# Performance work log

Measured on AMD Instinct MI355X. Metric: run time of the kernel, lower is better.

Reference implementation:

```python
import jax, jax.numpy as jnp
from jax import lax
import numpy as np

B, T, H, C = 64, 512, 1024, 21


def setup_inputs() -> dict:
    key = jax.random.key(0)
    k1, k2, k3, k4 = jax.random.split(key, 4)
    return {
        "sequence_output": jax.random.normal(k1, (B, T, H), dtype=jnp.float32),
        "input_mask": jax.random.randint(k2, (B, T), 0, 2, dtype=jnp.int32),
        "W": jax.random.normal(k3, (H, C), dtype=jnp.float32) * 0.02,
        "b": jnp.zeros((C,), dtype=jnp.float32),
        "transitions": jax.random.normal(k4, (C, C), dtype=jnp.float32) * 0.1,
    }


def crf_decode(logits, transitions, seq_len):
    """Viterbi decode matching tfa.text.crf_decode semantics (length-masked)."""
    Bb, Tt, Cc = logits.shape
    ident = jnp.arange(Cc, dtype=jnp.int32)[None, :]  # identity backpointers

    def fwd_step(state, inp):
        logit_t, t = inp  # [B,C], scalar step index
        scores = state[:, :, None] + transitions[None, :, :]  # [B, C_prev, C_cur]
        bp = jnp.argmax(scores, axis=1).astype(jnp.int32)      # [B, C]
        new_state = jnp.max(scores, axis=1) + logit_t          # [B, C]
        valid = (t < seq_len)[:, None]                          # [B, 1]
        state = jnp.where(valid, new_state, state)
        bp = jnp.where(valid, bp, ident)
        return state, bp

    ts = jnp.arange(1, Tt)
    xs = (jnp.transpose(logits[:, 1:], (1, 0, 2)), ts)
    final_state, bps = lax.scan(fwd_step, logits[:, 0], xs)  # bps: [T-1, B, C]
    last_tag = jnp.argmax(final_state, axis=-1).astype(jnp.int32)  # [B]

    def back_step(tag, bp_t):
        tag = jnp.take_along_axis(bp_t, tag[:, None], axis=1)[:, 0]
        return tag, tag

    _, tags_rev = lax.scan(back_step, last_tag, bps, reverse=True)  # [T-1, B]
    tags = jnp.concatenate([tags_rev, last_tag[None, :]], axis=0)   # [T, B]
    return jnp.transpose(tags, (1, 0))  # [B, T]


def reference(sequence_output, input_mask, W, b, transitions):
    # classifier logits
    logits = jnp.einsum("bth,hc->btc", sequence_output, W) + b  # [B,T,C]
    mask = (input_mask == 1).astype(jnp.int32)
    seq_len = jnp.sum(mask, axis=-1)  # [B]
    decode_tags = crf_decode(logits, transitions, seq_len)
    return jax.nn.one_hot(decode_tags, logits.shape[-1], dtype=jnp.float32), logits
```

## Files before the change

kernel.cpp:

```cpp
#include <hip/hip_runtime.h>
#include <stdint.h>

#define BB 64
#define TT 512
#define HH 1024
#define CC 21

#define GAS __attribute__((address_space(1)))
#define LAS __attribute__((address_space(3)))
__device__ __forceinline__ void gll16(const void* g, void* l) {
    __builtin_amdgcn_global_load_lds((const GAS uint32_t*)g, (LAS uint32_t*)l, 16, 0, 0);
}

#define RL(x, lane) __uint_as_float(__builtin_amdgcn_readlane(__float_as_uint(x), (lane)))

__global__ __launch_bounds__(512) void logits_kernel(
    const float* __restrict__ seq,
    const float* __restrict__ W,
    const float* __restrict__ bias,
    float* __restrict__ logits)
{
    __shared__ float comb[7][128][22];

    const int t = threadIdx.x;
    const int w = t >> 6;
    const int l = t & 63;
    const int row0 = blockIdx.x * 128;
    const int h0 = w * 128;

    const float* x0 = seq + (size_t)(row0 + l) * HH + h0;
    const float* x1 = seq + (size_t)(row0 + l + 64) * HH + h0;
    const float* wb = W + (size_t)h0 * CC;

    float acc0[CC], acc1[CC];
#pragma unroll
    for (int c = 0; c < CC; ++c) { acc0[c] = 0.f; acc1[c] = 0.f; }

    float4 xa[4], xbv[4], xan[4], xbn[4];
    float wr[6], wrn[6];

#pragma unroll
    for (int k = 0; k < 4; ++k) {
        xa[k]  = *(const float4*)(x0 + k * 4);
        xbv[k] = *(const float4*)(x1 + k * 4);
    }
#pragma unroll
    for (int i = 0; i < 6; ++i) {
        int j = i * 64 + l;
        wr[i] = (j < 16 * CC) ? wb[j] : 0.f;
    }

#pragma unroll 2
    for (int ch = 0; ch < 8; ++ch) {
        if (ch < 7) {
            const float* px0 = x0 + (ch + 1) * 16;
            const float* px1 = x1 + (ch + 1) * 16;
#pragma unroll
            for (int k = 0; k < 4; ++k) {
                xan[k] = *(const float4*)(px0 + k * 4);
                xbn[k] = *(const float4*)(px1 + k * 4);
            }
            const float* pw = wb + (ch + 1) * 16 * CC;
#pragma unroll
            for (int i = 0; i < 6; ++i) {
                int j = i * 64 + l;
                wrn[i] = (j < 16 * CC) ? pw[j] : 0.f;
            }
        }

#pragma unroll
        for (int g = 0; g < 4; ++g) {
#pragma unroll
            for (int j = 0; j < 4; ++j) {
                float xv0 = (&xa[g].x)[j];
                float xv1 = (&xbv[g].x)[j];
#pragma unroll
                for (int c = 0; c < CC; ++c) {
                    const int idx = (g * 4 + j) * CC + c;
                    float s = RL(wr[idx >> 6], idx & 63);
                    acc0[c] = fmaf(s, xv0, acc0[c]);
                    acc1[c] = fmaf(s, xv1, acc1[c]);
                }
            }
        }

        if (ch < 7) {
#pragma unroll
            for (int k = 0; k < 4; ++k) { xa[k] = xan[k]; xbv[k] = xbn[k]; }
#pragma unroll
            for (int i = 0; i < 6; ++i) wr[i] = wrn[i];
        }
    }

    if (w > 0) {
#pragma unroll
        for (int c = 0; c < CC; ++c) {
            comb[w - 1][l][c]      = acc0[c];
            comb[w - 1][l + 64][c] = acc1[c];
        }
    }
    __syncthreads();
    if (w == 0) {
        float* o0 = logits + (size_t)(row0 + l) * CC;
        float* o1 = logits + (size_t)(row0 + l + 64) * CC;
#pragma unroll
        for (int c = 0; c < CC; ++c) {
            float s0 = acc0[c] + bias[c];
            float s1 = acc1[c] + bias[c];
#pragma unroll
            for (int i = 0; i < 7; ++i) {
                s0 += comb[i][l][c];
                s1 += comb[i][l + 64][c];
            }
            o0[c] = s0;
            o1[c] = s1;
        }
    }
}

__global__ __launch_bounds__(256) void viterbi_kernel(
    const float* __restrict__ logits,
    const int* __restrict__ mask,
    const float* __restrict__ trans,
    float* __restrict__ onehot)
{
    __shared__ __align__(16) float lg[(TT + 1) * CC];
    __shared__ float stS[TT * CC];
    __shared__ float trL[CC * CC];
    __shared__ unsigned char bp[TT * CC];
    __shared__ unsigned char tagl[TT];
    __shared__ unsigned char mapl[12 * CC];
    __shared__ unsigned char bnd[13];

    const int tid = threadIdx.x;
    const int w = tid >> 6;
    const int l = tid & 63;
    const int b = blockIdx.x;

    const float* lb = logits + (size_t)b * TT * CC;
    for (int i = w; i < 42; i += 4)
        gll16(lb + (size_t)(i * 64 + l) * 4, &lg[i * 256]);

    for (int j = tid; j < CC * CC; j += 256) trL[j] = trans[j];

    int sl = 0;
#pragma unroll
    for (int k = 0; k < 8; ++k) sl += mask[b * TT + k * 64 + l];
#pragma unroll
    for (int o = 32; o > 0; o >>= 1) sl += __shfl_xor(sl, o);
    const int idstart = (sl >= 1) ? (sl - 1) : 0;

    asm volatile("s_waitcnt vmcnt(0)" ::: "memory");
    __syncthreads();

    if (w == 0) {
        const bool act = (l < CC);
        const int cc = act ? l : 0;
        float tcol[CC];
#pragma unroll
        for (int cp = 0; cp < CC; ++cp) tcol[cp] = trL[cp * CC + cc];

        float st = lg[cc];
        if (act) stS[l] = st;
        float lgt_next = lg[CC + cc];

#pragma unroll 1
        for (int t = 1; t < sl; ++t) {
            float lgt = lgt_next;
            lgt_next = lg[(t + 1) * CC + cc];
            float sc[CC];
#pragma unroll
            for (int cp = 0; cp < CC; ++cp) sc[cp] = RL(st, cp) + tcol[cp];
            float m0 = fmaxf(fmaxf(sc[0], sc[1]), sc[2]);
            float m1 = fmaxf(fmaxf(sc[3], sc[4]), sc[5]);
            float m2 = fmaxf(fmaxf(sc[6], sc[7]), sc[8]);
            float m3 = fmaxf(fmaxf(sc[9], sc[10]), sc[11]);
            float m4 = fmaxf(fmaxf(sc[12], sc[13]), sc[14]);
            float m5 = fmaxf(fmaxf(sc[15], sc[16]), sc[17]);
            float m6 = fmaxf(fmaxf(sc[18], sc[19]), sc[20]);
            float n0 = fmaxf(fmaxf(m0, m1), m2);
            float n1 = fmaxf(fmaxf(m3, m4), m5);
            float best = fmaxf(fmaxf(n0, n1), m6);
            st = best + lgt;
            if (act) stS[t * CC + l] = st;
        }

        float fs[CC];
#pragma unroll
        for (int cp = 0; cp < CC; ++cp) fs[cp] = RL(st, cp);
        float q0 = fmaxf(fmaxf(fs[0], fs[1]), fs[2]);
        float q1 = fmaxf(fmaxf(fs[3], fs[4]), fs[5]);
        float q2 = fmaxf(fmaxf(fs[6], fs[7]), fs[8]);
        float q3 = fmaxf(fmaxf(fs[9], fs[10]), fs[11]);
        float q4 = fmaxf(fmaxf(fs[12], fs[13]), fs[14]);
        float q5 = fmaxf(fmaxf(fs[15], fs[16]), fs[17]);
        float q6 = fmaxf(fmaxf(fs[18], fs[19]), fs[20]);
        float fbest = fmaxf(fmaxf(fmaxf(q0, q1), fmaxf(q2, q3)),
                            fmaxf(fmaxf(q4, q5), q6));
        int e[CC];
#pragma unroll
        for (int cp = 0; cp < CC; ++cp) e[cp] = (fs[cp] == fbest) ? cp : 63;
        int i0 = min(min(e[0], e[1]), e[2]);
        int i1 = min(min(e[3], e[4]), e[5]);
        int i2 = min(min(e[6], e[7]), e[8]);
        int i3 = min(min(e[9], e[10]), e[11]);
        int i4 = min(min(e[12], e[13]), e[14]);
        int i5 = min(min(e[15], e[16]), e[17]);
        int i6 = min(min(e[18], e[19]), e[20]);
        int last = min(min(min(i0, i1), min(i2, i3)), min(min(i4, i5), i6));
        if (l == 0) tagl[TT - 1] = (unsigned char)last;
    } else {
        int s = (w - 1) * 64 + l;
        if (s < 189) {
            int c0 = s % CC, prow = s / CC;
#pragma unroll 1
            for (int p = idstart + prow; p < TT; p += 9)
                bp[p * CC + c0] = (unsigned char)c0;
        }
    }
    __syncthreads();

    if (tid < 252) {
        const int c0 = tid % CC, tg = tid / CC;
        float tc[CC];
#pragma unroll
        for (int cp = 0; cp < CC; ++cp) tc[cp] = trL[cp * CC + c0];
#pragma unroll 1
        for (int t = 1 + tg; t < sl; t += 12) {
            const float* sp = stS + (t - 1) * CC;
            float bv = sp[0] + tc[0];
            int bi = 0;
#pragma unroll
            for (int cp = 1; cp < CC; ++cp) {
                float v = sp[cp] + tc[cp];
                bool g = v > bv;
                bv = g ? v : bv;
                bi = g ? cp : bi;
            }
            bp[(t - 1) * CC + c0] = (unsigned char)bi;
        }
    }
    __syncthreads();

    if (tid < 252) {
        int g = tid / CC, cand = tid % CC;
        int endp = g * 43;
        int startp = min(g * 43 + 42, TT - 2);
        int m = cand;
#pragma unroll 1
        for (int i = 0; i < 43; ++i) {
            int p = startp - i;
            int pr = (p >= endp) ? p : endp;
            int m2 = bp[pr * CC + m];
            m = (p >= endp) ? m2 : m;
        }
        mapl[g * CC + cand] = (unsigned char)m;
    }
    __syncthreads();

    if (tid == 0) {
        int eb = tagl[TT - 1];
        bnd[12] = (unsigned char)eb;
        for (int g = 11; g >= 0; --g) {
            eb = mapl[g * CC + eb];
            bnd[g] = (unsigned char)eb;
        }
    }
    __syncthreads();

    if (tid < 12) {
        int g = tid;
        int endp = g * 43;
        int startp = min(g * 43 + 42, TT - 2);
        int eb = bnd[g + 1];
#pragma unroll 1
        for (int p = startp; p >= endp; --p) {
            eb = bp[p * CC + eb];
            tagl[p] = (unsigned char)eb;
        }
    }
    __syncthreads();

    if (tid < 252) {
        const int c0 = tid % CC, prow = tid / CC;
        float* ob = onehot + (size_t)b * TT * CC;
#pragma unroll 1
        for (int p = prow; p < TT; p += 12)
            ob[(size_t)p * CC + c0] = (c0 == (int)tagl[p]) ? 1.f : 0.f;
    }
}

extern "C" void kernel_launch(void* const* d_in, const int* in_sizes, int n_in,
                              void* d_out, int out_size, void* d_ws, size_t ws_size,
                              hipStream_t stream) {
    const float* seq   = (const float*)d_in[0];
    const int*   msk   = (const int*)d_in[1];
    const float* W     = (const float*)d_in[2];
    const float* bias  = (const float*)d_in[3];
    const float* trans = (const float*)d_in[4];

    float* onehot_out = (float*)d_out;
    float* logits_out = onehot_out + (size_t)BB * TT * CC;

    logits_kernel<<<256, 512, 0, stream>>>(seq, W, bias, logits_out);
    viterbi_kernel<<<BB, 256, 0, stream>>>(logits_out, msk, trans, onehot_out);
}
```

Measured before the change: 135.0 us.

## Split logits GEMV across hidden halves and sum partials in viterbi kernel

The logits kernel now launches twice as many blocks, each covering half of the hidden dimension, so the GPU gets 512 workgroups instead of 256. The second half's partial sums go to a workspace buffer. The viterbi kernel loads both partials, adds them in LDS and writes the final logits out. This aims to improve CU utilisation for the bandwidth-bound GEMV. In exchange it adds extra global traffic for the partial buffer and more load work in the serial viterbi kernel. A fallback path runs the original kernel when the workspace is too small.

```diff
diff --git a/kernel.cpp b/kernel.cpp
--- a/kernel.cpp
+++ b/kernel.cpp
@@ -14,19 +14,22 @@
 
 #define RL(x, lane) __uint_as_float(__builtin_amdgcn_readlane(__float_as_uint(x), (lane)))
 
-__global__ __launch_bounds__(512) void logits_kernel(
+__global__ __launch_bounds__(512) void logits_split_kernel(
     const float* __restrict__ seq,
     const float* __restrict__ W,
     const float* __restrict__ bias,
-    float* __restrict__ logits)
+    float* __restrict__ outA,
+    float* __restrict__ outB)
 {
     __shared__ float comb[7][128][22];
 
     const int t = threadIdx.x;
     const int w = t >> 6;
     const int l = t & 63;
-    const int row0 = blockIdx.x * 128;
-    const int h0 = w * 128;
+    const int r  = blockIdx.x >> 1;
+    const int hb = blockIdx.x & 1;
+    const int row0 = r * 128;
+    const int h0 = hb * 512 + w * 64;
 
     const float* x0 = seq + (size_t)(row0 + l) * HH + h0;
     const float* x1 = seq + (size_t)(row0 + l + 64) * HH + h0;
@@ -51,8 +54,8 @@
     }
 
 #pragma unroll 2
-    for (int ch = 0; ch < 8; ++ch) {
-        if (ch < 7) {
+    for (int ch = 0; ch < 4; ++ch) {
+        if (ch < 3) {
             const float* px0 = x0 + (ch + 1) * 16;
             const float* px1 = x1 + (ch + 1) * 16;
 #pragma unroll
@@ -84,7 +87,7 @@
             }
         }
 
-        if (ch < 7) {
+        if (ch < 3) {
 #pragma unroll
             for (int k = 0; k < 4; ++k) { xa[k] = xan[k]; xbv[k] = xbn[k]; }
 #pragma unroll
@@ -101,6 +104,103 @@
     }
     __syncthreads();
     if (w == 0) {
+        float* dst = hb ? outB : outA;
+        float* o0 = dst + (size_t)(row0 + l) * CC;
+        float* o1 = dst + (size_t)(row0 + l + 64) * CC;
+#pragma unroll
+        for (int c = 0; c < CC; ++c) {
+            float s0 = acc0[c] + (hb ? 0.f : bias[c]);
+            float s1 = acc1[c] + (hb ? 0.f : bias[c]);
+#pragma unroll
+            for (int i = 0; i < 7; ++i) {
+                s0 += comb[i][l][c];
+                s1 += comb[i][l + 64][c];
+            }
+            o0[c] = s0;
+            o1[c] = s1;
+        }
+    }
+}
+
+__global__ __launch_bounds__(512) void logits_full_kernel(
+    const float* __restrict__ seq, const float* __restrict__ W,
+    const float* __restrict__ bias, float* __restrict__ logits)
+{
+    __shared__ float comb[7][128][22];
+    const int t = threadIdx.x;
+    const int w = t >> 6;
+    const int l = t & 63;
+    const int row0 = blockIdx.x * 128;
+    const int h0 = w * 128;
+
+    const float* x0 = seq + (size_t)(row0 + l) * HH + h0;
+    const float* x1 = seq + (size_t)(row0 + l + 64) * HH + h0;
+    const float* wb = W + (size_t)h0 * CC;
+
+    float acc0[CC], acc1[CC];
+#pragma unroll
+    for (int c = 0; c < CC; ++c) { acc0[c] = 0.f; acc1[c] = 0.f; }
+
+    float4 xa[4], xbv[4], xan[4], xbn[4];
+    float wr[6], wrn[6];
+#pragma unroll
+    for (int k = 0; k < 4; ++k) {
+        xa[k]  = *(const float4*)(x0 + k * 4);
+        xbv[k] = *(const float4*)(x1 + k * 4);
+    }
+#pragma unroll
+    for (int i = 0; i < 6; ++i) {
+        int j = i * 64 + l;
+        wr[i] = (j < 16 * CC) ? wb[j] : 0.f;
+    }
+#pragma unroll 2
+    for (int ch = 0; ch < 8; ++ch) {
+        if (ch < 7) {
+            const float* px0 = x0 + (ch + 1) * 16;
+            const float* px1 = x1 + (ch + 1) * 16;
+#pragma unroll
+            for (int k = 0; k < 4; ++k) {
+                xan[k] = *(const float4*)(px0 + k * 4);
+                xbn[k] = *(const float4*)(px1 + k * 4);
+            }
+            const float* pw = wb + (ch + 1) * 16 * CC;
+#pragma unroll
+            for (int i = 0; i < 6; ++i) {
+                int j = i * 64 + l;
+                wrn[i] = (j < 16 * CC) ? pw[j] : 0.f;
+            }
+        }
+#pragma unroll
+        for (int g = 0; g < 4; ++g) {
+#pragma unroll
+            for (int j = 0; j < 4; ++j) {
+                float xv0 = (&xa[g].x)[j];
+                float xv1 = (&xbv[g].x)[j];
+#pragma unroll
+                for (int c = 0; c < CC; ++c) {
+                    const int idx = (g * 4 + j) * CC + c;
+                    float s = RL(wr[idx >> 6], idx & 63);
+                    acc0[c] = fmaf(s, xv0, acc0[c]);
+                    acc1[c] = fmaf(s, xv1, acc1[c]);
+                }
+            }
+        }
+        if (ch < 7) {
+#pragma unroll
+            for (int k = 0; k < 4; ++k) { xa[k] = xan[k]; xbv[k] = xbn[k]; }
+#pragma unroll
+            for (int i = 0; i < 6; ++i) wr[i] = wrn[i];
+        }
+    }
+    if (w > 0) {
+#pragma unroll
+        for (int c = 0; c < CC; ++c) {
+            comb[w - 1][l][c]      = acc0[c];
+            comb[w - 1][l + 64][c] = acc1[c];
+        }
+    }
+    __syncthreads();
+    if (w == 0) {
         float* o0 = logits + (size_t)(row0 + l) * CC;
         float* o1 = logits + (size_t)(row0 + l + 64) * CC;
 #pragma unroll
@@ -119,10 +219,12 @@
 }
 
 __global__ __launch_bounds__(256) void viterbi_kernel(
-    const float* __restrict__ logits,
+    const float* __restrict__ logitsA,
+    const float* __restrict__ logitsB,
     const int* __restrict__ mask,
     const float* __restrict__ trans,
-    float* __restrict__ onehot)
+    float* __restrict__ onehot,
+    float* __restrict__ logits_out)
 {
     __shared__ __align__(16) float lg[(TT + 1) * CC];
     __shared__ float stS[TT * CC];
@@ -137,10 +239,20 @@
     const int l = tid & 63;
     const int b = blockIdx.x;
 
-    const float* lb = logits + (size_t)b * TT * CC;
+    const float* lb = logitsA + (size_t)b * TT * CC;
     for (int i = w; i < 42; i += 4)
         gll16(lb + (size_t)(i * 64 + l) * 4, &lg[i * 256]);
 
+    float4 bfr[11];
+    if (logitsB) {
+        const float4* pb = (const float4*)(logitsB + (size_t)b * TT * CC);
+#pragma unroll
+        for (int k = 0; k < 11; ++k) {
+            int j = tid + k * 256;
+            bfr[k] = (j < 2688) ? pb[j] : float4{0.f, 0.f, 0.f, 0.f};
+        }
+    }
+
     for (int j = tid; j < CC * CC; j += 256) trL[j] = trans[j];
 
     int sl = 0;
@@ -152,6 +264,23 @@
 
     asm volatile("s_waitcnt vmcnt(0)" ::: "memory");
     __syncthreads();
+
+    if (logitsB) {
+        float4* lg4 = (float4*)lg;
+        float4* gout = (float4*)(logits_out + (size_t)b * TT * CC);
+#pragma unroll
+        for (int k = 0; k < 11; ++k) {
+            int j = tid + k * 256;
+            if (j < 2688) {
+                float4 a = lg4[j];
+                a.x += bfr[k].x; a.y += bfr[k].y;
+                a.z += bfr[k].z; a.w += bfr[k].w;
+                lg4[j] = a;
+                gout[j] = a;
+            }
+        }
+        __syncthreads();
+    }
 
     if (w == 0) {
         const bool act = (l < CC);
@@ -302,6 +431,16 @@
     float* onehot_out = (float*)d_out;
     float* logits_out = onehot_out + (size_t)BB * TT * CC;
 
-    logits_kernel<<<256, 512, 0, stream>>>(seq, W, bias, logits_out);
-    viterbi_kernel<<<BB, 256, 0, stream>>>(logits_out, msk, trans, onehot_out);
+    const size_t bbytes = (size_t)BB * TT * CC * sizeof(float);
+    if (ws_size >= bbytes) {
+        float* partB = (float*)d_ws;
+        logits_split_kernel<<<512, 512, 0, stream>>>(seq, W, bias,
+                                                     logits_out, partB);
+        viterbi_kernel<<<BB, 256, 0, stream>>>(logits_out, partB, msk, trans,
+                                               onehot_out, logits_out);
+    } else {
+        logits_full_kernel<<<256, 512, 0, stream>>>(seq, W, bias, logits_out);
+        viterbi_kernel<<<BB, 256, 0, stream>>>(logits_out, nullptr, msk, trans,
+                                               onehot_out, logits_out);
+    }
 }
```

Result: slower. 152.1 us (+12.7%).
